# Kernel optimization log

Hardware: AMD Instinct MI355X
Metric: run time of the kernel (lower is better)

## Reference

```python
import jax, jax.numpy as jnp
import numpy as np

B, N, H = 32, 2048, 128
L4H = 4 * H  # concatenated (c0,h0,c1,h1) embedding dim


def _lstm_cell(x, c, h, Wx, Wh, b):
    g = x @ Wx + h @ Wh + b                      # [B,N,4H]
    i, f, gg, o = jnp.split(g, 4, axis=-1)
    c_new = jax.nn.sigmoid(f) * c + jax.nn.sigmoid(i) * jnp.tanh(gg)
    h_new = jax.nn.sigmoid(o) * jnp.tanh(c_new)
    return c_new, h_new


def setup_inputs() -> dict:
    key = jax.random.key(0)
    ks = jax.random.split(key, 20)
    s = 0.05
    inp = {
        'node_embeddings': jax.random.normal(ks[0], (B, N, H), jnp.float32),
        'c0': jax.random.normal(ks[1], (B, N, H), jnp.float32),
        'h0': jax.random.normal(ks[2], (B, N, H), jnp.float32),
        'c1': jax.random.normal(ks[3], (B, N, H), jnp.float32),
        'h1': jax.random.normal(ks[4], (B, N, H), jnp.float32),
        'instruction_pointer': jax.random.uniform(ks[5], (B, N), jnp.float32),
        'Wx0': s * jax.random.normal(ks[6], (H, 4 * H), jnp.float32),
        'Wh0': s * jax.random.normal(ks[7], (H, 4 * H), jnp.float32),
        'b0': jnp.zeros((4 * H,), jnp.float32),
        'Wx1': s * jax.random.normal(ks[8], (H, 4 * H), jnp.float32),
        'Wh1': s * jax.random.normal(ks[9], (H, 4 * H), jnp.float32),
        'b1': jnp.zeros((4 * H,), jnp.float32),
        'raise_W': s * jax.random.normal(ks[10], (L4H, 2), jnp.float32),
        'raise_b': jnp.zeros((2,), jnp.float32),
        'branch_W': s * jax.random.normal(ks[11], (L4H, 2), jnp.float32),
        'branch_b': jnp.zeros((2,), jnp.float32),
        'true_indexes': jax.random.randint(ks[12], (B, N), 0, N, jnp.int32),
        'false_indexes': jax.random.randint(ks[13], (B, N), 0, N, jnp.int32),
        'raise_indexes': jax.random.randint(ks[14], (B, N), 0, N, jnp.int32),
        'exit_node_indexes': jax.random.randint(ks[15], (B,), 0, N, jnp.int32),
        'raise_node_indexes': jax.random.randint(ks[16], (B,), 0, N, jnp.int32),
        'current_step': jnp.zeros((B,), jnp.int32),
        'step_limits': jax.random.randint(ks[17], (B,), 1, 100, jnp.int32),
    }
    return inp


def reference(node_embeddings, c0, h0, c1, h1, instruction_pointer,
              Wx0, Wh0, b0, Wx1, Wh1, b1, raise_W, raise_b, branch_W, branch_b,
              true_indexes, false_indexes, raise_indexes,
              exit_node_indexes, raise_node_indexes, current_step, step_limits):
    num_nodes = node_embeddings.shape[1]

    # --- execute: stacked 2-layer LSTM per node (vectorized over B,N) ---
    c0n, h0n = _lstm_cell(node_embeddings, c0, h0, Wx0, Wh0, b0)
    c1n, h1n = _lstm_cell(h0n, c1, h1, Wx1, Wh1, b1)
    old = (c0, h0, c1, h1)
    contrib = (c0n, h0n, c1n, h1n)

    # --- mask exit and raise nodes: keep old hidden state there ---
    node_ids = jnp.arange(num_nodes)[None, :]                  # [1,N]
    m_exit = node_ids == exit_node_indexes[:, None]            # [B,N]
    m_raise = node_ids == raise_node_indexes[:, None]          # [B,N]
    m_keep = (m_exit | m_raise)[..., None]                     # raise_in_ipagnn=True
    contrib = tuple(jnp.where(m_keep, o, c) for o, c in zip(old, contrib))

    # --- raise / branch decisions ---
    emb = jnp.concatenate(contrib, axis=-1)                    # [B,N,4H]
    raise_dec = jax.nn.softmax(emb @ raise_W + raise_b, axis=-1)
    raise_dec = jnp.where(m_exit[..., None], jnp.array([0.0, 1.0], raise_dec.dtype), raise_dec)
    branch_dec = jax.nn.softmax(emb @ branch_W + branch_b, axis=-1)

    p_raise = raise_dec[..., 0]
    p_noraise = raise_dec[..., 1]
    p_true = p_noraise * branch_dec[..., 0]
    p_false = p_noraise * branch_dec[..., 1]

    seg = jax.vmap(lambda d, i: jax.ops.segment_sum(d, i, num_segments=num_nodes))

    # --- instruction pointer update (scatter-add over soft edges) ---
    ip = instruction_pointer
    ip_new = (seg(p_raise * ip, raise_indexes)
              + seg(p_true * ip, true_indexes)
              + seg(p_false * ip, false_indexes))               # [B,N]

    # --- hidden-state aggregation, weighted by instruction pointer ---
    denom = (ip_new + 1e-7)[..., None]                          # [B,N,1]
    wr = (p_raise * ip)[..., None]
    wt = (p_true * ip)[..., None]
    wf = (p_false * ip)[..., None]
    agg = tuple((seg(hc * wr, raise_indexes)
                 + seg(hc * wt, true_indexes)
                 + seg(hc * wf, false_indexes)) / denom
                for hc in contrib)

    # --- keep old state if example already hit its step limit ---
    live = (current_step < step_limits)                         # [B]
    ip_fin = jnp.where(live[:, None], ip_new, ip)
    hid_fin = tuple(jnp.where(live[:, None, None], a, o) for a, o in zip(agg, old))

    # pack carry: (c0,h0,c1,h1) embedding + instruction pointer -> [B,N,4H+1]
    return jnp.concatenate(list(hid_fin) + [ip_fin[..., None]], axis=-1)
```

## Files before the change

### kernel.cpp

```cpp
#include <hip/hip_runtime.h>
#include <hip/hip_bf16.h>

constexpr int Bc  = 32;
constexpr int Nc  = 2048;
constexpr int Hc  = 128;
constexpr int H4c = 512;
constexpr int BNc = Bc * Nc;

typedef __attribute__((ext_vector_type(8))) short short8;
typedef __attribute__((ext_vector_type(4))) float f32x4;

__device__ __forceinline__ float sigf(float x)  { return 1.f / (1.f + __expf(-x)); }
__device__ __forceinline__ float tanh_(float x) { return 1.f - 2.f / (__expf(2.f * x) + 1.f); }

__device__ __forceinline__ unsigned short bfu(float f) {
    union { float f; unsigned u; } a; a.f = f;
    unsigned u = a.u;
    return (unsigned short)((u + 0x7FFFu + ((u >> 16) & 1u)) >> 16);
}
__device__ __forceinline__ float bf2f(unsigned short u) {
    union { unsigned u; float f; } a; a.u = ((unsigned)u) << 16;
    return a.f;
}
__device__ __forceinline__ unsigned cvtpk(float lo, float hi) {
    unsigned r;
    asm("v_cvt_pk_bf16_f32 %0, %1, %2" : "=v"(r) : "v"(lo), "v"(hi));
    return r;
}

__device__ __forceinline__ int a_off(int buf, int row, int byte) {
    return buf * 5120 + row * 80 + byte;
}
__device__ __forceinline__ int cs_off(int row, int unit) {
    return row * 512 + ((unit ^ (row & 7)) << 4);
}

__global__ __launch_bounds__(256) void prep_kernel(
    const float* __restrict__ Wx0, const float* __restrict__ Wh0,
    const float* __restrict__ Wx1, const float* __restrict__ Wh1,
    unsigned short* __restrict__ W0F, unsigned short* __restrict__ W1F)
{
    int idx = blockIdx.x * 256 + threadIdx.x;
    int ct = idx >> 9, ks = (idx >> 6) & 7, lane = idx & 63;
    int col = ct * 16 + (lane & 15);
    unsigned short* p0 = W0F + (size_t)idx * 8;
    unsigned short* p1 = W1F + (size_t)idx * 8;
    #pragma unroll
    for (int e = 0; e < 8; ++e) {
        int k = ks * 32 + (lane >> 4) * 8 + e;
        float v0 = (k < 128) ? Wx0[k * 512 + col] : Wh0[(k - 128) * 512 + col];
        float v1 = (k < 128) ? Wx1[k * 512 + col] : Wh1[(k - 128) * 512 + col];
        p0[e] = bfu(v0);
        p1[e] = bfu(v1);
    }
}

__global__ __launch_bounds__(512, 4) void gemm0_kernel(
    const float* __restrict__ x_in,  const float* __restrict__ c0_in,
    const float* __restrict__ h0_in, const float* __restrict__ h1_in,
    const unsigned short* __restrict__ W0F, const float* __restrict__ b0,
    const int* __restrict__ exit_i, const int* __restrict__ raise_i,
    unsigned short* __restrict__ contrib, unsigned short* __restrict__ A1F)
{
    __shared__ __align__(16) char Ab[10240];
    __shared__ __align__(16) char Cs[32768];

    const int t    = threadIdx.x;
    const int w    = t >> 6, l = t & 63, lr = l & 15, lg = l >> 4;
    const int row0 = blockIdx.x * 64;
    const int bidx = row0 >> 11;
    const int eb   = exit_i[bidx];
    const int rbn  = raise_i[bidx];
    const int j    = w * 16 + lr;

    const int srow = t >> 3, sfq = t & 7;
#define STAGE0(c, bi)                                                          \
    {                                                                          \
        const float* sp = ((c) < 4 ? x_in : h0_in)                             \
            + (size_t)(row0 + srow) * Hc + ((c) & 3) * 32 + sfq * 4;           \
        float4 v = *(const float4*)sp;                                         \
        uint2 b2 = { cvtpk(v.x, v.y), cvtpk(v.z, v.w) };                       \
        *(uint2*)(Ab + a_off(bi, srow, sfq * 8)) = b2;                         \
    }

    f32x4 acc[4][4];
    #pragma unroll
    for (int g = 0; g < 4; ++g) {
        float bv = b0[g * 128 + j];
        f32x4 vv = {bv, bv, bv, bv};
        #pragma unroll
        for (int mt = 0; mt < 4; ++mt) acc[mt][g] = vv;
    }

    STAGE0(0, 0);
    short8 bn[4];
    #pragma unroll
    for (int g = 0; g < 4; ++g)
        bn[g] = *(const short8*)(W0F + ((size_t)((g * 8 + w) * 8) * 64 + l) * 8);
    #pragma unroll
    for (int c = 0; c < 8; ++c) {
        __syncthreads();
        short8 bc[4];
        #pragma unroll
        for (int g = 0; g < 4; ++g) bc[g] = bn[g];
        if (c < 7) {
            STAGE0(c + 1, (c + 1) & 1);
            #pragma unroll
            for (int g = 0; g < 4; ++g)
                bn[g] = *(const short8*)(W0F + ((size_t)((g * 8 + w) * 8 + c + 1) * 64 + l) * 8);
        }
        short8 a[4];
        #pragma unroll
        for (int mt = 0; mt < 4; ++mt)
            a[mt] = *(const short8*)(Ab + a_off(c & 1, mt * 16 + lr, lg * 16));
        #pragma unroll
        for (int mt = 0; mt < 4; ++mt)
            #pragma unroll
            for (int g = 0; g < 4; ++g)
                acc[mt][g] = __builtin_amdgcn_mfma_f32_16x16x32_bf16(
                    a[mt], bc[g], acc[mt][g], 0, 0, 0);
    }

    unsigned hnp[4][4];
    #pragma unroll
    for (int mt = 0; mt < 4; ++mt) {
        #pragma unroll
        for (int rr = 0; rr < 4; ++rr) {
            const int row  = mt * 16 + lg * 4 + rr;
            const int grow = row0 + row;
            const int n    = grow & (Nc - 1);
            float cold = c0_in[(size_t)grow * Hc + j];
            float h1f  = h1_in[(size_t)grow * Hc + j];
            float ig = sigf(acc[mt][0][rr]);
            float fg = sigf(acc[mt][1][rr]);
            float gv = tanh_(acc[mt][2][rr]);
            float og = sigf(acc[mt][3][rr]);
            float cn = fg * cold + ig * gv;
            float hn = og * tanh_(cn);
            const bool keep = (n == eb) || (n == rbn);
            float cw = keep ? cold : cn;
            float hw = hn;
            if (keep) hw = h0_in[(size_t)grow * Hc + j];
            float cwn = __shfl_xor(cw, 1);
            float hwn = __shfl_xor(hw, 1);
            if (!(lr & 1)) {
                *(unsigned*)(Cs + cs_off(row, j >> 3) + (j & 7) * 2)        = cvtpk(cw, cwn);
                *(unsigned*)(Cs + cs_off(row, 16 + (j >> 3)) + (j & 7) * 2) = cvtpk(hw, hwn);
            }
            hnp[mt][rr] = cvtpk(hn, h1f);
        }
    }
    __syncthreads();
    #pragma unroll
    for (int i = 0; i < 4; ++i) {
        const int idx = i * 512 + t;
        const int r = idx >> 5, u = idx & 31;
        short8 v = *(const short8*)(Cs + cs_off(r, u));
        *(short8*)(contrib + (size_t)(row0 + r) * H4c + u * 8) = v;
    }
    __syncthreads();
    #pragma unroll
    for (int mt = 0; mt < 4; ++mt)
        #pragma unroll
        for (int rr = 0; rr < 4; ++rr) {
            const int row = mt * 16 + lg * 4 + rr;
            unsigned pn = __shfl_xor(hnp[mt][rr], 1);
            if (!(lr & 1)) {
                unsigned h0d = (hnp[mt][rr] & 0xFFFFu) | (pn << 16);
                unsigned h1d = (hnp[mt][rr] >> 16) | (pn & 0xFFFF0000u);
                *(unsigned*)(Cs + cs_off(row, j >> 3) + (j & 7) * 2)        = h0d;
                *(unsigned*)(Cs + cs_off(row, 16 + (j >> 3)) + (j & 7) * 2) = h1d;
            }
        }
    __syncthreads();
    #pragma unroll
    for (int i = 0; i < 4; ++i) {
        const int idx  = i * 512 + t;
        const int frag = idx >> 6;
        const int lane = idx & 63;
        const int mt = frag >> 3, ks = frag & 7;
        const int row  = mt * 16 + (lane & 15);
        const int unit = ks * 4 + (lane >> 4);
        short8 v = *(const short8*)(Cs + cs_off(row, unit));
        *(short8*)(A1F + (((size_t)blockIdx.x * 32 + frag) << 9) + (size_t)lane * 8) = v;
    }
#undef STAGE0
}

__global__ __launch_bounds__(512, 4) void gemm1_kernel(
    const unsigned short* __restrict__ A1F, const float* __restrict__ c1_in,
    const float* __restrict__ h1_in,
    const unsigned short* __restrict__ W1F, const float* __restrict__ b1,
    const float* __restrict__ rW, const float* __restrict__ rbv,
    const float* __restrict__ bW, const float* __restrict__ bbv,
    const float* __restrict__ ip_in,
    const int* __restrict__ exit_i, const int* __restrict__ raise_i,
    unsigned short* __restrict__ contrib, float* __restrict__ w_all)
{
    __shared__ __align__(16) char Cs[32768];
    __shared__ __align__(16) float dw[2048];

    const int t    = threadIdx.x;
    const int w    = t >> 6, l = t & 63, lr = l & 15, lg = l >> 4;
    const int row0 = blockIdx.x * 64;
    const int bidx = row0 >> 11;
    const int eb   = exit_i[bidx];
    const int rbn  = raise_i[bidx];
    const int j    = w * 16 + lr;

    if (t < 256) {
        ((float4*)dw)[t]       = ((const float4*)rW)[t];
        ((float4*)dw)[256 + t] = ((const float4*)bW)[t];
    }

    f32x4 acc[4][4];
    #pragma unroll
    for (int g = 0; g < 4; ++g) {
        float bv = b1[g * 128 + j];
        f32x4 vv = {bv, bv, bv, bv};
        #pragma unroll
        for (int mt = 0; mt < 4; ++mt) acc[mt][g] = vv;
    }

    const unsigned short* Af = A1F + ((size_t)blockIdx.x * 32 << 9);
    #pragma unroll
    for (int ks = 0; ks < 8; ++ks) {
        short8 a[4], b[4];
        #pragma unroll
        for (int mt = 0; mt < 4; ++mt)
            a[mt] = *(const short8*)(Af + (((size_t)(mt * 8 + ks)) << 9) + (size_t)l * 8);
        #pragma unroll
        for (int g = 0; g < 4; ++g)
            b[g] = *(const short8*)(W1F + ((size_t)((g * 8 + w) * 8 + ks) * 64 + l) * 8);
        #pragma unroll
        for (int mt = 0; mt < 4; ++mt)
            #pragma unroll
            for (int g = 0; g < 4; ++g)
                acc[mt][g] = __builtin_amdgcn_mfma_f32_16x16x32_bf16(
                    a[mt], b[g], acc[mt][g], 0, 0, 0);
    }

    #pragma unroll
    for (int mt = 0; mt < 4; ++mt) {
        #pragma unroll
        for (int rr = 0; rr < 4; ++rr) {
            const int row  = mt * 16 + lg * 4 + rr;
            const int grow = row0 + row;
            const int n    = grow & (Nc - 1);
            float cold = c1_in[(size_t)grow * Hc + j];
            float ig = sigf(acc[mt][0][rr]);
            float fg = sigf(acc[mt][1][rr]);
            float gv = tanh_(acc[mt][2][rr]);
            float og = sigf(acc[mt][3][rr]);
            float cn = fg * cold + ig * gv;
            float hn = og * tanh_(cn);
            const bool keep = (n == eb) || (n == rbn);
            float cw = keep ? cold : cn;
            float hw = hn;
            if (keep) hw = h1_in[(size_t)grow * Hc + j];
            float cwn = __shfl_xor(cw, 1);
            float hwn = __shfl_xor(hw, 1);
            if (!(lr & 1)) {
                *(unsigned*)(Cs + cs_off(row, j >> 3) + (j & 7) * 2)        = cvtpk(cw, cwn);
                *(unsigned*)(Cs + cs_off(row, 16 + (j >> 3)) + (j & 7) * 2) = cvtpk(hw, hwn);
            }
        }
    }
    __syncthreads();

    #pragma unroll
    for (int i = 0; i < 4; ++i) {
        const int idx = i * 512 + t;
        const int r = idx >> 5, u = idx & 31;
        short8 v = *(const short8*)(Cs + cs_off(r, u));
        *(short8*)(contrib + (size_t)(row0 + r) * H4c + 256 + u * 8) = v;
    }

    {
        const int r8 = l >> 3, s = l & 7;
        const int row  = w * 8 + r8;
        const int grow = row0 + row;
        float pr0 = 0.f, pr1 = 0.f, pb0 = 0.f, pb1 = 0.f;
        #pragma unroll
        for (int cu = 0; cu < 8; ++cu) {
            short8 ev;
            if (s < 4)
                ev = *(const short8*)(contrib + (size_t)grow * H4c + s * 64 + cu * 8);
            else
                ev = *(const short8*)(Cs + cs_off(row, (s - 4) * 8 + cu));
            const int col0 = s * 64 + cu * 8;
            const float4* rp = (const float4*)(dw + col0 * 2);
            const float4* bp = (const float4*)(dw + 1024 + col0 * 2);
            #pragma unroll
            for (int q = 0; q < 4; ++q) {
                float4 rv = rp[q], bv = bp[q];
                float e0 = bf2f((unsigned short)ev[q * 2]);
                float e1 = bf2f((unsigned short)ev[q * 2 + 1]);
                pr0 += e0 * rv.x + e1 * rv.z;
                pr1 += e0 * rv.y + e1 * rv.w;
                pb0 += e0 * bv.x + e1 * bv.z;
                pb1 += e0 * bv.y + e1 * bv.w;
            }
        }
        #pragma unroll
        for (int m = 1; m < 8; m <<= 1) {
            pr0 += __shfl_xor(pr0, m);
            pr1 += __shfl_xor(pr1, m);
            pb0 += __shfl_xor(pb0, m);
            pb1 += __shfl_xor(pb1, m);
        }
        if (s == 0) {
            const int n = grow & (Nc - 1);
            float r0v = pr0 + rbv[0], r1v = pr1 + rbv[1];
            float m  = fmaxf(r0v, r1v);
            float z0 = __expf(r0v - m), z1 = __expf(r1v - m);
            float inv = 1.f / (z0 + z1);
            float praise = z0 * inv, pno = z1 * inv;
            if (n == eb) { praise = 0.f; pno = 1.f; }
            float q0 = pb0 + bbv[0], q1 = pb1 + bbv[1];
            float mm = fmaxf(q0, q1);
            float y0 = __expf(q0 - mm), y1 = __expf(q1 - mm);
            float binv = 1.f / (y0 + y1);
            float ipv = ip_in[grow];
            w_all[grow]            = praise * ipv;
            w_all[BNc + grow]      = pno * y0 * binv * ipv;
            w_all[2 * BNc + grow]  = pno * y1 * binv * ipv;
        }
    }
}

__global__ __launch_bounds__(256) void build_kernel(
    const int* __restrict__ t_idx, const int* __restrict__ f_idx,
    const int* __restrict__ r_idx, int* __restrict__ head, int* __restrict__ nxt)
{
    const int row  = blockIdx.x * 256 + threadIdx.x;
    const int base = (row >> 11) << 11;
    const int e0 = row * 4;
    int o;
    o = atomicExch(&head[base + r_idx[row]], e0);     nxt[e0]     = o;
    o = atomicExch(&head[base + t_idx[row]], e0 + 1); nxt[e0 + 1] = o;
    o = atomicExch(&head[base + f_idx[row]], e0 + 2); nxt[e0 + 2] = o;
}

__global__ __launch_bounds__(256) void gather_kernel(
    const unsigned short* __restrict__ contrib, const float* __restrict__ w_all,
    const int* __restrict__ head, const int* __restrict__ nxt,
    const float* __restrict__ c0_in, const float* __restrict__ h0_in,
    const float* __restrict__ c1_in, const float* __restrict__ h1_in,
    const float* __restrict__ ip_in,
    const int* __restrict__ cstep, const int* __restrict__ slim,
    float* __restrict__ out)
{
    const int gtid = blockIdx.x * 256 + threadIdx.x;
    const int wid  = gtid >> 6;
    const int l    = gtid & 63;
    const int bidx = wid >> 11;

    float acc[8] = {0.f, 0.f, 0.f, 0.f, 0.f, 0.f, 0.f, 0.f};
    float ipsum = 0.f;

    int e = head[wid];
    while (e >= 0) {
        const int src = e >> 2;
        const float w = w_all[(e & 3) * BNc + src];
        const unsigned short* crow = contrib + (size_t)src * 512;
        #pragma unroll
        for (int q = 0; q < 8; ++q) acc[q] += w * bf2f(crow[q * 64 + l]);
        ipsum += w;
        e = nxt[e];
    }

    const bool live = cstep[bidx] < slim[bidx];
    float* orow = out + (size_t)wid * 513;
    if (live) {
        const float inv = 1.f / (ipsum + 1e-7f);
        #pragma unroll
        for (int q = 0; q < 8; ++q) orow[q * 64 + l] = acc[q] * inv;
        if (l == 0) orow[512] = ipsum;
    } else {
        #pragma unroll
        for (int q = 0; q < 8; ++q) {
            const int off = (q & 1) * 64 + l;
            const float* p = (q >> 1) == 0 ? c0_in : (q >> 1) == 1 ? h0_in
                           : (q >> 1) == 2 ? c1_in : h1_in;
            orow[q * 64 + l] = p[(size_t)wid * Hc + off];
        }
        if (l == 0) orow[512] = ip_in[wid];
    }
}

extern "C" void kernel_launch(void* const* d_in, const int* in_sizes, int n_in,
                              void* d_out, int out_size, void* d_ws, size_t ws_size,
                              hipStream_t stream) {
    const float* x     = (const float*)d_in[0];
    const float* c0    = (const float*)d_in[1];
    const float* h0    = (const float*)d_in[2];
    const float* c1    = (const float*)d_in[3];
    const float* h1    = (const float*)d_in[4];
    const float* ip    = (const float*)d_in[5];
    const float* Wx0   = (const float*)d_in[6];
    const float* Wh0   = (const float*)d_in[7];
    const float* b0    = (const float*)d_in[8];
    const float* Wx1   = (const float*)d_in[9];
    const float* Wh1   = (const float*)d_in[10];
    const float* b1    = (const float*)d_in[11];
    const float* rW    = (const float*)d_in[12];
    const float* rb    = (const float*)d_in[13];
    const float* bW    = (const float*)d_in[14];
    const float* bb    = (const float*)d_in[15];
    const int* t_idx   = (const int*)d_in[16];
    const int* f_idx   = (const int*)d_in[17];
    const int* r_idx   = (const int*)d_in[18];
    const int* exit_i  = (const int*)d_in[19];
    const int* raise_i = (const int*)d_in[20];
    const int* cstep   = (const int*)d_in[21];
    const int* slim    = (const int*)d_in[22];
    float* out = (float*)d_out;

    unsigned short* contrib = (unsigned short*)d_ws;
    unsigned short* A1F = contrib + (size_t)BNc * 512;
    unsigned short* W0F = A1F + (size_t)BNc * 256;
    unsigned short* W1F = W0F + 512 * 256;
    float* w_all = (float*)(W1F + 512 * 256);
    int*   head  = (int*)(w_all + 3 * (size_t)BNc);
    int*   nxt   = head + BNc;

    hipMemsetAsync(head, 0xFF, BNc * sizeof(int), stream);

    prep_kernel<<<64, 256, 0, stream>>>(Wx0, Wh0, Wx1, Wh1, W0F, W1F);
    gemm0_kernel<<<BNc / 64, 512, 0, stream>>>(x, c0, h0, h1, W0F, b0,
                                               exit_i, raise_i, contrib, A1F);
    gemm1_kernel<<<BNc / 64, 512, 0, stream>>>(A1F, c1, h1, W1F, b1,
                                               rW, rb, bW, bb, ip,
                                               exit_i, raise_i, contrib, w_all);
    build_kernel<<<BNc / 256, 256, 0, stream>>>(t_idx, f_idx, r_idx, head, nxt);
    gather_kernel<<<BNc / 4, 256, 0, stream>>>(contrib, w_all, head, nxt,
                                               c0, h0, c1, h1, ip, cstep, slim, out);
}
```

Before: 214.3 us.

## Drop the A1F intermediate and stage layer-1 inputs from contrib and h1

gemm0 no longer writes a separate pre-fragmented bf16 layer-1 input buffer (A1F) and no longer reads h1. gemm1 now builds its A operand itself through a double-buffered LDS pipeline, reading the new h0 half from the bf16 contrib buffer and converting fp32 h1 on the fly, the same way gemm0 stages its inputs. This removes a full write and re-read of the intermediate buffer, at the cost of LDS staging and barriers in gemm1. Two smaller changes ride along: the LDS writes for the packed output switch from paired shuffle-and-pack stores to per-element 16-bit stores, and the routing-weight scratch reuses the staging buffer. One risk: layer 1 now reads the masked h written to contrib (the original h0 at exit and raise nodes) rather than the raw layer-0 output.

```diff
diff --git a/kernel.cpp b/kernel.cpp
--- a/kernel.cpp
+++ b/kernel.cpp
@@ -57,10 +57,10 @@
 
 __global__ __launch_bounds__(512, 4) void gemm0_kernel(
     const float* __restrict__ x_in,  const float* __restrict__ c0_in,
-    const float* __restrict__ h0_in, const float* __restrict__ h1_in,
+    const float* __restrict__ h0_in,
     const unsigned short* __restrict__ W0F, const float* __restrict__ b0,
     const int* __restrict__ exit_i, const int* __restrict__ raise_i,
-    unsigned short* __restrict__ contrib, unsigned short* __restrict__ A1F)
+    unsigned short* __restrict__ contrib)
 {
     __shared__ __align__(16) char Ab[10240];
     __shared__ __align__(16) char Cs[32768];
@@ -121,7 +121,6 @@
                     a[mt], bc[g], acc[mt][g], 0, 0, 0);
     }
 
-    unsigned hnp[4][4];
     #pragma unroll
     for (int mt = 0; mt < 4; ++mt) {
         #pragma unroll
@@ -130,7 +129,6 @@
             const int grow = row0 + row;
             const int n    = grow & (Nc - 1);
             float cold = c0_in[(size_t)grow * Hc + j];
-            float h1f  = h1_in[(size_t)grow * Hc + j];
             float ig = sigf(acc[mt][0][rr]);
             float fg = sigf(acc[mt][1][rr]);
             float gv = tanh_(acc[mt][2][rr]);
@@ -141,13 +139,8 @@
             float cw = keep ? cold : cn;
             float hw = hn;
             if (keep) hw = h0_in[(size_t)grow * Hc + j];
-            float cwn = __shfl_xor(cw, 1);
-            float hwn = __shfl_xor(hw, 1);
-            if (!(lr & 1)) {
-                *(unsigned*)(Cs + cs_off(row, j >> 3) + (j & 7) * 2)        = cvtpk(cw, cwn);
-                *(unsigned*)(Cs + cs_off(row, 16 + (j >> 3)) + (j & 7) * 2) = cvtpk(hw, hwn);
-            }
-            hnp[mt][rr] = cvtpk(hn, h1f);
+            *(unsigned short*)(Cs + cs_off(row, j >> 3) + (j & 7) * 2)        = bfu(cw);
+            *(unsigned short*)(Cs + cs_off(row, 16 + (j >> 3)) + (j & 7) * 2) = bfu(hw);
         }
     }
     __syncthreads();
@@ -158,37 +151,11 @@
         short8 v = *(const short8*)(Cs + cs_off(r, u));
         *(short8*)(contrib + (size_t)(row0 + r) * H4c + u * 8) = v;
     }
-    __syncthreads();
-    #pragma unroll
-    for (int mt = 0; mt < 4; ++mt)
-        #pragma unroll
-        for (int rr = 0; rr < 4; ++rr) {
-            const int row = mt * 16 + lg * 4 + rr;
-            unsigned pn = __shfl_xor(hnp[mt][rr], 1);
-            if (!(lr & 1)) {
-                unsigned h0d = (hnp[mt][rr] & 0xFFFFu) | (pn << 16);
-                unsigned h1d = (hnp[mt][rr] >> 16) | (pn & 0xFFFF0000u);
-                *(unsigned*)(Cs + cs_off(row, j >> 3) + (j & 7) * 2)        = h0d;
-                *(unsigned*)(Cs + cs_off(row, 16 + (j >> 3)) + (j & 7) * 2) = h1d;
-            }
-        }
-    __syncthreads();
-    #pragma unroll
-    for (int i = 0; i < 4; ++i) {
-        const int idx  = i * 512 + t;
-        const int frag = idx >> 6;
-        const int lane = idx & 63;
-        const int mt = frag >> 3, ks = frag & 7;
-        const int row  = mt * 16 + (lane & 15);
-        const int unit = ks * 4 + (lane >> 4);
-        short8 v = *(const short8*)(Cs + cs_off(row, unit));
-        *(short8*)(A1F + (((size_t)blockIdx.x * 32 + frag) << 9) + (size_t)lane * 8) = v;
-    }
 #undef STAGE0
 }
 
 __global__ __launch_bounds__(512, 4) void gemm1_kernel(
-    const unsigned short* __restrict__ A1F, const float* __restrict__ c1_in,
+    const unsigned short* __restrict__ contrib_r, const float* __restrict__ c1_in,
     const float* __restrict__ h1_in,
     const unsigned short* __restrict__ W1F, const float* __restrict__ b1,
     const float* __restrict__ rW, const float* __restrict__ rbv,
@@ -197,8 +164,8 @@
     const int* __restrict__ exit_i, const int* __restrict__ raise_i,
     unsigned short* __restrict__ contrib, float* __restrict__ w_all)
 {
+    __shared__ __align__(16) char Ab[10240];
     __shared__ __align__(16) char Cs[32768];
-    __shared__ __align__(16) float dw[2048];
 
     const int t    = threadIdx.x;
     const int w    = t >> 6, l = t & 63, lr = l & 15, lg = l >> 4;
@@ -208,9 +175,20 @@
     const int rbn  = raise_i[bidx];
     const int j    = w * 16 + lr;
 
-    if (t < 256) {
-        ((float4*)dw)[t]       = ((const float4*)rW)[t];
-        ((float4*)dw)[256 + t] = ((const float4*)bW)[t];
+    const int srow = t >> 3, sfq = t & 7;
+#define STAGE1(c, bi)                                                          \
+    {                                                                          \
+        if ((c) < 4) {                                                         \
+            ushort4 v = *(const ushort4*)(contrib_r                            \
+                + (size_t)(row0 + srow) * H4c + 128 + ((c) & 3) * 32 + sfq * 4); \
+            *(ushort4*)(Ab + a_off(bi, srow, sfq * 8)) = v;                    \
+        } else {                                                               \
+            const float* sp = h1_in + (size_t)(row0 + srow) * Hc               \
+                + ((c) & 3) * 32 + sfq * 4;                                    \
+            float4 v = *(const float4*)sp;                                     \
+            uint2 b2 = { cvtpk(v.x, v.y), cvtpk(v.z, v.w) };                   \
+            *(uint2*)(Ab + a_off(bi, srow, sfq * 8)) = b2;                     \
+        }                                                                      \
     }
 
     f32x4 acc[4][4];
@@ -222,22 +200,33 @@
         for (int mt = 0; mt < 4; ++mt) acc[mt][g] = vv;
     }
 
-    const unsigned short* Af = A1F + ((size_t)blockIdx.x * 32 << 9);
-    #pragma unroll
-    for (int ks = 0; ks < 8; ++ks) {
-        short8 a[4], b[4];
+    STAGE1(0, 0);
+    short8 bn[4];
+    #pragma unroll
+    for (int g = 0; g < 4; ++g)
+        bn[g] = *(const short8*)(W1F + ((size_t)((g * 8 + w) * 8) * 64 + l) * 8);
+    #pragma unroll
+    for (int c = 0; c < 8; ++c) {
+        __syncthreads();
+        short8 bc[4];
+        #pragma unroll
+        for (int g = 0; g < 4; ++g) bc[g] = bn[g];
+        if (c < 7) {
+            STAGE1(c + 1, (c + 1) & 1);
+            #pragma unroll
+            for (int g = 0; g < 4; ++g)
+                bn[g] = *(const short8*)(W1F + ((size_t)((g * 8 + w) * 8 + c + 1) * 64 + l) * 8);
+        }
+        short8 a[4];
         #pragma unroll
         for (int mt = 0; mt < 4; ++mt)
-            a[mt] = *(const short8*)(Af + (((size_t)(mt * 8 + ks)) << 9) + (size_t)l * 8);
-        #pragma unroll
-        for (int g = 0; g < 4; ++g)
-            b[g] = *(const short8*)(W1F + ((size_t)((g * 8 + w) * 8 + ks) * 64 + l) * 8);
+            a[mt] = *(const short8*)(Ab + a_off(c & 1, mt * 16 + lr, lg * 16));
         #pragma unroll
         for (int mt = 0; mt < 4; ++mt)
             #pragma unroll
             for (int g = 0; g < 4; ++g)
                 acc[mt][g] = __builtin_amdgcn_mfma_f32_16x16x32_bf16(
-                    a[mt], b[g], acc[mt][g], 0, 0, 0);
+                    a[mt], bc[g], acc[mt][g], 0, 0, 0);
     }
 
     #pragma unroll
@@ -258,16 +247,17 @@
             float cw = keep ? cold : cn;
             float hw = hn;
             if (keep) hw = h1_in[(size_t)grow * Hc + j];
-            float cwn = __shfl_xor(cw, 1);
-            float hwn = __shfl_xor(hw, 1);
-            if (!(lr & 1)) {
-                *(unsigned*)(Cs + cs_off(row, j >> 3) + (j & 7) * 2)        = cvtpk(cw, cwn);
-                *(unsigned*)(Cs + cs_off(row, 16 + (j >> 3)) + (j & 7) * 2) = cvtpk(hw, hwn);
-            }
+            *(unsigned short*)(Cs + cs_off(row, j >> 3) + (j & 7) * 2)        = bfu(cw);
+            *(unsigned short*)(Cs + cs_off(row, 16 + (j >> 3)) + (j & 7) * 2) = bfu(hw);
         }
     }
     __syncthreads();
-
+    float* dw = (float*)Ab;
+    if (t < 256) {
+        ((float4*)dw)[t]       = ((const float4*)rW)[t];
+        ((float4*)dw)[256 + t] = ((const float4*)bW)[t];
+    }
+    __syncthreads();
     #pragma unroll
     for (int i = 0; i < 4; ++i) {
         const int idx = i * 512 + t;
@@ -285,7 +275,7 @@
         for (int cu = 0; cu < 8; ++cu) {
             short8 ev;
             if (s < 4)
-                ev = *(const short8*)(contrib + (size_t)grow * H4c + s * 64 + cu * 8);
+                ev = *(const short8*)(contrib_r + (size_t)grow * H4c + s * 64 + cu * 8);
             else
                 ev = *(const short8*)(Cs + cs_off(row, (s - 4) * 8 + cu));
             const int col0 = s * 64 + cu * 8;
@@ -327,6 +317,7 @@
             w_all[2 * BNc + grow]  = pno * y1 * binv * ipv;
         }
     }
+#undef STAGE1
 }
 
 __global__ __launch_bounds__(256) void build_kernel(
@@ -418,8 +409,7 @@
     float* out = (float*)d_out;
 
     unsigned short* contrib = (unsigned short*)d_ws;
-    unsigned short* A1F = contrib + (size_t)BNc * 512;
-    unsigned short* W0F = A1F + (size_t)BNc * 256;
+    unsigned short* W0F = contrib + (size_t)BNc * 512;
     unsigned short* W1F = W0F + 512 * 256;
     float* w_all = (float*)(W1F + 512 * 256);
     int*   head  = (int*)(w_all + 3 * (size_t)BNc);
@@ -428,9 +418,9 @@
     hipMemsetAsync(head, 0xFF, BNc * sizeof(int), stream);
 
     prep_kernel<<<64, 256, 0, stream>>>(Wx0, Wh0, Wx1, Wh1, W0F, W1F);
-    gemm0_kernel<<<BNc / 64, 512, 0, stream>>>(x, c0, h0, h1, W0F, b0,
-                                               exit_i, raise_i, contrib, A1F);
-    gemm1_kernel<<<BNc / 64, 512, 0, stream>>>(A1F, c1, h1, W1F, b1,
+    gemm0_kernel<<<BNc / 64, 512, 0, stream>>>(x, c0, h0, W0F, b0,
+                                               exit_i, raise_i, contrib);
+    gemm1_kernel<<<BNc / 64, 512, 0, stream>>>(contrib, c1, h1, W1F, b1,
                                                rW, rb, bW, bb, ip,
                                                exit_i, raise_i, contrib, w_all);
     build_kernel<<<BNc / 256, 256, 0, stream>>>(t_idx, f_idx, r_idx, head, nxt);
```

Measured after the change: 199.6 us. 1.07x faster.
